# Performance work log

Measured on AMD Instinct MI355X. Metric: run time of the kernel, lower is better.

## Reference

```python
import jax, jax.numpy as jnp
import numpy as np

FP4_E2M1_VALUES = [0.0, 0.0625, 8.0, 1.0, 2.0, 3.0, 4.0, 6.0,
                   -0.0, -0.0625, -8.0, -1.0, -2.0, -3.0, -4.0, -6.0]

M, N, K = 4096, 4096, 4096


def setup_inputs() -> dict:
    key = jax.random.key(0)
    k1, k2 = jax.random.split(key)
    x = jax.random.normal(k1, (M, K), dtype=jnp.float16)
    # packed uint8 bytes stored as int32 (values in [0,256)); each byte holds
    # two fp4 indices: high nibble = even k, low nibble = odd k
    packed_weight = jax.random.randint(k2, (N, K // 2), 0, 256, dtype=jnp.int32)
    lut = jnp.array(FP4_E2M1_VALUES, dtype=jnp.float16)
    return {"x": x, "packed_weight": packed_weight, "lut": lut}


def reference(x, packed_weight, lut):
    # Dequantize: unpack nibbles along K, LUT lookup -> W [N, K] fp16
    n, kh = packed_weight.shape
    high = (packed_weight >> 4) & 15   # even k positions
    low = packed_weight & 15           # odd k positions
    idx = jnp.stack([high, low], axis=-1).reshape(n, 2 * kh)  # [N, K]
    w = lut[idx]                       # [N, K] fp16
    # GEMM with fp32 accumulation (Triton kernel accumulates in fp32), cast to fp16
    y = jnp.einsum('mk,nk->mn', x, w, preferred_element_type=jnp.float32)
    return y.astype(jnp.float16)
```

## Files before the change

kernel.cpp:

```cpp
#include <hip/hip_runtime.h>
#include <hip/hip_fp16.h>
#include <stdint.h>

#define M_DIM 4096
#define N_DIM 4096
#define K_DIM 4096
#define BM 128
#define BN 128
#define BK 32
#define KW (K_DIM / 2)
#define WS_XH_BYTES ((size_t)M_DIM * K_DIM * 2)
#define WS_WH_BYTES ((size_t)N_DIM * K_DIM * 2)

typedef _Float16 half8 __attribute__((ext_vector_type(8)));
typedef float f32x4 __attribute__((ext_vector_type(4)));

__device__ __forceinline__ uint32_t pk2(float a, float b) {
  auto h = __builtin_amdgcn_cvt_pkrtz(a, b);
  return __builtin_bit_cast(uint32_t, h);
}

__device__ __forceinline__ uint32_t dq(uint32_t b, uint32_t ph, uint32_t pl) {
#if __has_builtin(__builtin_amdgcn_perm)
  const uint32_t sel = ((b & 0x70u) << 4) | ((b & 0x07u) << 24);
  uint32_t v = __builtin_amdgcn_perm(ph, pl, sel);
#else
  const uint64_t pool = ((uint64_t)ph << 32) | pl;
  const uint32_t mh = (uint32_t)(pool >> (((b >> 4) & 7u) * 8)) & 0xFFu;
  const uint32_t ml = (uint32_t)(pool >> ((b & 7u) * 8)) & 0xFFu;
  uint32_t v = (mh << 8) | (ml << 24);
#endif
  const uint32_t sg = ((b & 0x88u) * 0x10000100u) & 0x80008000u;
  return v | sg;
}

__device__ __forceinline__ void lut_pool(const float* __restrict__ lutf,
                                         uint32_t& ph, uint32_t& pl) {
  const uint32_t h01 = pk2(lutf[0], lutf[1]);
  const uint32_t h23 = pk2(lutf[2], lutf[3]);
  const uint32_t h45 = pk2(lutf[4], lutf[5]);
  const uint32_t h67 = pk2(lutf[6], lutf[7]);
#if __has_builtin(__builtin_amdgcn_perm)
  pl = __builtin_amdgcn_perm(h23, h01, 0x07050301u);
  ph = __builtin_amdgcn_perm(h67, h45, 0x07050301u);
#else
  pl = ((h01 >> 8) & 0xFFu) | ((h01 >> 24) << 8) |
       (((h23 >> 8) & 0xFFu) << 16) | ((h23 >> 24) << 24);
  ph = ((h45 >> 8) & 0xFFu) | ((h45 >> 24) << 8) |
       (((h67 >> 8) & 0xFFu) << 16) | ((h67 >> 24) << 24);
#endif
}

__global__ __launch_bounds__(256) void cvt_x_kernel(const float4* __restrict__ xin,
                                                    uint4* __restrict__ xout) {
  const int i = blockIdx.x * 256 + threadIdx.x;
  const float4 v0 = xin[2 * i];
  const float4 v1 = xin[2 * i + 1];
  xout[i] = make_uint4(pk2(v0.x, v0.y), pk2(v0.z, v0.w),
                       pk2(v1.x, v1.y), pk2(v1.z, v1.w));
}

__global__ __launch_bounds__(256) void wdq_kernel(const int4* __restrict__ pin,
                                                  uint4* __restrict__ wout,
                                                  const float* __restrict__ lutf) {
  uint32_t ph, pl;
  lut_pool(lutf, ph, pl);
  const int i = blockIdx.x * 256 + threadIdx.x;
  const int4 w = pin[i];
  wout[i] = make_uint4(dq(w.x, ph, pl), dq(w.y, ph, pl),
                       dq(w.z, ph, pl), dq(w.w, ph, pl));
}

__global__ __launch_bounds__(256, 2) void f16gemm_kernel(
    const uint8_t* __restrict__ xh,
    const uint8_t* __restrict__ wh,
    float* __restrict__ out)
{
  __shared__ uint16_t ldsA[BM * BK];
  __shared__ uint16_t ldsB[BN * BK];

  const int tid  = threadIdx.x;
  const int lane = tid & 63;
  const int wave = tid >> 6;
  const int wm   = wave >> 1;
  const int wn   = wave & 1;
  const int m0 = blockIdx.y * BM;
  const int n0 = blockIdx.x * BN;

  f32x4 acc[4][4];
#pragma unroll
  for (int i = 0; i < 4; ++i)
#pragma unroll
    for (int j = 0; j < 4; ++j) acc[i][j] = (f32x4){0.f, 0.f, 0.f, 0.f};

  const uint8_t* xbase = xh + (size_t)m0 * K_DIM * 2;
  const uint8_t* wbase = wh + (size_t)n0 * K_DIM * 2;

  for (int kt = 0; kt < K_DIM / BK; ++kt) {
    __syncthreads();

#pragma unroll
    for (int s = 0; s < 2; ++s) {
      const int idx = tid + s * 256;
      const int row = idx >> 2;
      const int c16 = idx & 3;
      const int g16 = c16 ^ ((row >> 1) & 3);
      const size_t goff = ((size_t)row * K_DIM + kt * BK) * 2 + g16 * 16;
      __builtin_amdgcn_global_load_lds(
          (const __attribute__((address_space(1))) uint32_t*)(xbase + goff),
          (__attribute__((address_space(3))) uint32_t*)((uint8_t*)ldsA + (size_t)idx * 16),
          16, 0, 0);
      __builtin_amdgcn_global_load_lds(
          (const __attribute__((address_space(1))) uint32_t*)(wbase + goff),
          (__attribute__((address_space(3))) uint32_t*)((uint8_t*)ldsB + (size_t)idx * 16),
          16, 0, 0);
    }

    __syncthreads();

    const int q = lane >> 4;
    half8 af[4], bfr[4];
#pragma unroll
    for (int i = 0; i < 4; ++i) {
      const int row = wm * 64 + i * 16 + (lane & 15);
      const uint16_t* pa = ldsA + row * BK + (q ^ ((row >> 1) & 3)) * 8;
      af[i] = *(const half8*)pa;
    }
#pragma unroll
    for (int j = 0; j < 4; ++j) {
      const int row = wn * 64 + j * 16 + (lane & 15);
      const uint16_t* pb = ldsB + row * BK + (q ^ ((row >> 1) & 3)) * 8;
      bfr[j] = *(const half8*)pb;
    }
#pragma unroll
    for (int i = 0; i < 4; ++i)
#pragma unroll
      for (int j = 0; j < 4; ++j)
        acc[i][j] = __builtin_amdgcn_mfma_f32_16x16x32_f16(af[i], bfr[j], acc[i][j], 0, 0, 0);
  }

  const int mb = m0 + wm * 64 + (lane >> 4) * 4;
  const int nb = n0 + wn * 64 + (lane & 15);
#pragma unroll
  for (int i = 0; i < 4; ++i)
#pragma unroll
    for (int j = 0; j < 4; ++j)
#pragma unroll
      for (int r = 0; r < 4; ++r)
        out[(size_t)(mb + i * 16 + r) * N_DIM + (nb + j * 16)] = acc[i][j][r];
}

__global__ __launch_bounds__(256, 2) void fp4gemm_kernel(
    const uint8_t* __restrict__ xh,
    const int* __restrict__ pw,
    const float* __restrict__ lutf,
    float* __restrict__ out)
{
  __shared__ uint16_t ldsA[BM * BK];
  __shared__ uint16_t ldsB[BN * BK];

  const int tid  = threadIdx.x;
  const int lane = tid & 63;
  const int wave = tid >> 6;
  const int wm   = wave >> 1;
  const int wn   = wave & 1;
  const int m0 = blockIdx.y * BM;
  const int n0 = blockIdx.x * BN;

  uint32_t ph, pl;
  lut_pool(lutf, ph, pl);

  f32x4 acc[4][4];
#pragma unroll
  for (int i = 0; i < 4; ++i)
#pragma unroll
    for (int j = 0; j < 4; ++j) acc[i][j] = (f32x4){0.f, 0.f, 0.f, 0.f};

  const int rowB  = tid >> 1;
  const int halfB = tid & 1;
  const int swzB  = (rowB >> 1) & 3;

  for (int kt = 0; kt < K_DIM / BK; ++kt) {
    __syncthreads();

#pragma unroll
    for (int s = 0; s < 2; ++s) {
      const int idx = tid + s * 256;
      const int row = idx >> 2;
      const int c16 = idx & 3;
      const int g16 = c16 ^ ((row >> 1) & 3);
      const uint8_t* gp = xh + ((size_t)(m0 + row) * K_DIM + kt * BK) * 2 + g16 * 16;
      uint8_t* lp = (uint8_t*)ldsA + (size_t)idx * 16;
      __builtin_amdgcn_global_load_lds(
          (const __attribute__((address_space(1))) uint32_t*)gp,
          (__attribute__((address_space(3))) uint32_t*)lp, 16, 0, 0);
    }

    {
      const int* gp = pw + (size_t)(n0 + rowB) * KW + kt * (BK / 2) + halfB * 8;
      const int4 wA = ((const int4*)gp)[0];
      const int4 wB = ((const int4*)gp)[1];
      uint8_t* base = (uint8_t*)ldsB + rowB * 64;
      *(uint4*)(base + ((halfB * 2 + 0) ^ swzB) * 16) =
          make_uint4(dq(wA.x, ph, pl), dq(wA.y, ph, pl),
                     dq(wA.z, ph, pl), dq(wA.w, ph, pl));
      *(uint4*)(base + ((halfB * 2 + 1) ^ swzB) * 16) =
          make_uint4(dq(wB.x, ph, pl), dq(wB.y, ph, pl),
                     dq(wB.z, ph, pl), dq(wB.w, ph, pl));
    }

    __syncthreads();

    const int q = lane >> 4;
    half8 af[4], bfr[4];
#pragma unroll
    for (int i = 0; i < 4; ++i) {
      const int row = wm * 64 + i * 16 + (lane & 15);
      const uint16_t* pa = ldsA + row * BK + (q ^ ((row >> 1) & 3)) * 8;
      af[i] = *(const half8*)pa;
    }
#pragma unroll
    for (int j = 0; j < 4; ++j) {
      const int row = wn * 64 + j * 16 + (lane & 15);
      const uint16_t* pb = ldsB + row * BK + (q ^ ((row >> 1) & 3)) * 8;
      bfr[j] = *(const half8*)pb;
    }
#pragma unroll
    for (int i = 0; i < 4; ++i)
#pragma unroll
      for (int j = 0; j < 4; ++j)
        acc[i][j] = __builtin_amdgcn_mfma_f32_16x16x32_f16(af[i], bfr[j], acc[i][j], 0, 0, 0);
  }

  const int mb = m0 + wm * 64 + (lane >> 4) * 4;
  const int nb = n0 + wn * 64 + (lane & 15);
#pragma unroll
  for (int i = 0; i < 4; ++i)
#pragma unroll
    for (int j = 0; j < 4; ++j)
#pragma unroll
      for (int r = 0; r < 4; ++r)
        out[(size_t)(mb + i * 16 + r) * N_DIM + (nb + j * 16)] = acc[i][j][r];
}

extern "C" void kernel_launch(void* const* d_in, const int* in_sizes, int n_in,
                              void* d_out, int out_size, void* d_ws, size_t ws_size,
                              hipStream_t stream) {
  const void* px = nullptr; const void* ppw = nullptr; const void* plut = nullptr;
  for (int i = 0; i < n_in; ++i) {
    const long s = in_sizes[i];
    if (s == (long)M_DIM * K_DIM) px = d_in[i];
    else if (s == (long)N_DIM * KW) ppw = d_in[i];
    else if (s == 16) plut = d_in[i];
  }
  if (!px || !ppw || !plut) { px = d_in[0]; ppw = d_in[1]; plut = d_in[2]; }

  dim3 grid(N_DIM / BN, M_DIM / BM);

  cvt_x_kernel<<<(M_DIM * K_DIM / 8) / 256, 256, 0, stream>>>(
      (const float4*)px, (uint4*)d_ws);

  if (ws_size >= WS_XH_BYTES + WS_WH_BYTES) {
    uint8_t* wh = (uint8_t*)d_ws + WS_XH_BYTES;
    wdq_kernel<<<(N_DIM * KW / 4) / 256, 256, 0, stream>>>(
        (const int4*)ppw, (uint4*)wh, (const float*)plut);
    f16gemm_kernel<<<grid, dim3(256), 0, stream>>>(
        (const uint8_t*)d_ws, wh, (float*)d_out);
  } else {
    fp4gemm_kernel<<<grid, dim3(256), 0, stream>>>(
        (const uint8_t*)d_ws, (const int*)ppw, (const float*)plut, (float*)d_out);
  }
}
```

Measured before the change: 295.8 us.

## Replace fp16 GEMM with 256x256 tile, double-buffered, pipelined 8-wave kernel

```diff
diff --git a/kernel.cpp b/kernel.cpp
--- a/kernel.cpp
+++ b/kernel.cpp
@@ -5,9 +5,6 @@
 #define M_DIM 4096
 #define N_DIM 4096
 #define K_DIM 4096
-#define BM 128
-#define BN 128
-#define BK 32
 #define KW (K_DIM / 2)
 #define WS_XH_BYTES ((size_t)M_DIM * K_DIM * 2)
 #define WS_WH_BYTES ((size_t)N_DIM * K_DIM * 2)
@@ -71,90 +68,183 @@
                        dq(w.z, ph, pl), dq(w.w, ph, pl));
 }
 
-__global__ __launch_bounds__(256, 2) void f16gemm_kernel(
+__device__ __forceinline__ f32x4 mfma16(half8 a, half8 b, f32x4 c) {
+  return __builtin_amdgcn_mfma_f32_16x16x32_f16(a, b, c, 0, 0, 0);
+}
+
+#define NT (K_DIM / 64)
+
+__global__ __launch_bounds__(512, 2) void f16gemm256_kernel(
     const uint8_t* __restrict__ xh,
     const uint8_t* __restrict__ wh,
     float* __restrict__ out)
 {
-  __shared__ uint16_t ldsA[BM * BK];
-  __shared__ uint16_t ldsB[BN * BK];
+  __shared__ uint16_t Al[2][2][256 * 32];
+  __shared__ uint16_t Bl[2][2][256 * 32];
 
   const int tid  = threadIdx.x;
   const int lane = tid & 63;
   const int wave = tid >> 6;
-  const int wm   = wave >> 1;
-  const int wn   = wave & 1;
-  const int m0 = blockIdx.y * BM;
-  const int n0 = blockIdx.x * BN;
-
-  f32x4 acc[4][4];
-#pragma unroll
-  for (int i = 0; i < 4; ++i)
+  const int wm   = wave >> 2;
+  const int wn   = wave & 3;
+
+  const int bid = blockIdx.x;
+  const int sw  = (bid & 7) * 32 + (bid >> 3);
+  const int m0  = (sw >> 4) * 256;
+  const int n0  = (sw & 15) * 256;
+
+  const uint8_t* asrc[2];
+  const uint8_t* bsrc[2];
+  int ldst[2];
+#pragma unroll
+  for (int s = 0; s < 2; ++s) {
+    const int slot = tid + s * 512;
+    const int row  = slot >> 2;
+    const int g    = (slot & 3) ^ ((row >> 1) & 3);
+    asrc[s] = xh + ((size_t)(m0 + row) * K_DIM) * 2 + g * 16;
+    bsrc[s] = wh + ((size_t)(n0 + row) * K_DIM) * 2 + g * 16;
+    ldst[s] = slot * 16;
+  }
+
+  auto STAGE = [&](int isB, int buf, int kh, int tt) {
+    const int koff  = tt * 128 + kh * 64;
+    uint8_t* lb = (uint8_t*)(isB ? &Bl[0][0][0] : &Al[0][0][0]) +
+                  (buf * 2 + kh) * 16384;
+#pragma unroll
+    for (int s = 0; s < 2; ++s) {
+      const uint8_t* gp = (isB ? bsrc[s] : asrc[s]) + koff;
+      __builtin_amdgcn_global_load_lds(
+          (const __attribute__((address_space(1))) uint32_t*)gp,
+          (__attribute__((address_space(3))) uint32_t*)(lb + ldst[s]), 16, 0, 0);
+    }
+  };
+
+  int aoff[8], boff[4];
+#pragma unroll
+  for (int m = 0; m < 8; ++m) {
+    const int row = wm * 128 + m * 16 + (lane & 15);
+    const int ch  = (lane >> 4) ^ ((row >> 1) & 3);
+    aoff[m] = row * 32 + ch * 8;
+  }
+#pragma unroll
+  for (int n = 0; n < 4; ++n) {
+    const int row = wn * 64 + n * 16 + (lane & 15);
+    const int ch  = (lane >> 4) ^ ((row >> 1) & 3);
+    boff[n] = row * 32 + ch * 8;
+  }
+
+  f32x4 acc[8][4];
+#pragma unroll
+  for (int i = 0; i < 8; ++i)
 #pragma unroll
     for (int j = 0; j < 4; ++j) acc[i][j] = (f32x4){0.f, 0.f, 0.f, 0.f};
 
-  const uint8_t* xbase = xh + (size_t)m0 * K_DIM * 2;
-  const uint8_t* wbase = wh + (size_t)n0 * K_DIM * 2;
-
-  for (int kt = 0; kt < K_DIM / BK; ++kt) {
-    __syncthreads();
-
-#pragma unroll
-    for (int s = 0; s < 2; ++s) {
-      const int idx = tid + s * 256;
-      const int row = idx >> 2;
-      const int c16 = idx & 3;
-      const int g16 = c16 ^ ((row >> 1) & 3);
-      const size_t goff = ((size_t)row * K_DIM + kt * BK) * 2 + g16 * 16;
-      __builtin_amdgcn_global_load_lds(
-          (const __attribute__((address_space(1))) uint32_t*)(xbase + goff),
-          (__attribute__((address_space(3))) uint32_t*)((uint8_t*)ldsA + (size_t)idx * 16),
-          16, 0, 0);
-      __builtin_amdgcn_global_load_lds(
-          (const __attribute__((address_space(1))) uint32_t*)(wbase + goff),
-          (__attribute__((address_space(3))) uint32_t*)((uint8_t*)ldsB + (size_t)idx * 16),
-          16, 0, 0);
-    }
-
-    __syncthreads();
-
-    const int q = lane >> 4;
-    half8 af[4], bfr[4];
-#pragma unroll
-    for (int i = 0; i < 4; ++i) {
-      const int row = wm * 64 + i * 16 + (lane & 15);
-      const uint16_t* pa = ldsA + row * BK + (q ^ ((row >> 1) & 3)) * 8;
-      af[i] = *(const half8*)pa;
-    }
-#pragma unroll
-    for (int j = 0; j < 4; ++j) {
-      const int row = wn * 64 + j * 16 + (lane & 15);
-      const uint16_t* pb = ldsB + row * BK + (q ^ ((row >> 1) & 3)) * 8;
-      bfr[j] = *(const half8*)pb;
-    }
-#pragma unroll
-    for (int i = 0; i < 4; ++i)
-#pragma unroll
-      for (int j = 0; j < 4; ++j)
-        acc[i][j] = __builtin_amdgcn_mfma_f32_16x16x32_f16(af[i], bfr[j], acc[i][j], 0, 0, 0);
-  }
-
-  const int mb = m0 + wm * 64 + (lane >> 4) * 4;
+  STAGE(1, 0, 0, 0);
+  STAGE(0, 0, 0, 0);
+  STAGE(1, 0, 1, 0);
+  STAGE(0, 0, 1, 0);
+  STAGE(1, 1, 0, 1);
+  STAGE(0, 1, 0, 1);
+  asm volatile("s_waitcnt vmcnt(8)" ::: "memory");
+  __builtin_amdgcn_s_barrier();
+
+  half8 af[4], bfr[4];
+
+#pragma unroll 2
+  for (int t = 0; t < NT; ++t) {
+    const int cur = t & 1;
+    const uint16_t* Ab = &Al[cur][0][0];
+    const uint16_t* Bb = &Bl[cur][0][0];
+    const bool st1 = (t + 1 < NT);
+    const bool st2 = (t + 2 < NT);
+
+#pragma unroll
+    for (int n = 0; n < 4; ++n) bfr[n] = *(const half8*)(Bb + boff[n]);
+#pragma unroll
+    for (int m = 0; m < 4; ++m) af[m] = *(const half8*)(Ab + aoff[m]);
+    if (st1) STAGE(1, cur ^ 1, 1, t + 1);
+    __builtin_amdgcn_s_barrier();
+    asm volatile("s_waitcnt lgkmcnt(0)" ::: "memory");
+    __builtin_amdgcn_sched_barrier(0);
+    __builtin_amdgcn_s_setprio(1);
+#pragma unroll
+    for (int m = 0; m < 4; ++m)
+#pragma unroll
+      for (int n = 0; n < 4; ++n)
+        acc[m][n] = mfma16(af[m], bfr[n], acc[m][n]);
+    __builtin_amdgcn_s_setprio(0);
+    __builtin_amdgcn_s_barrier();
+
+#pragma unroll
+    for (int m = 0; m < 4; ++m) af[m] = *(const half8*)(Ab + aoff[4 + m]);
+    if (st1) STAGE(0, cur ^ 1, 1, t + 1);
+    __builtin_amdgcn_s_barrier();
+    asm volatile("s_waitcnt lgkmcnt(0)" ::: "memory");
+    __builtin_amdgcn_sched_barrier(0);
+    __builtin_amdgcn_s_setprio(1);
+#pragma unroll
+    for (int m = 0; m < 4; ++m)
+#pragma unroll
+      for (int n = 0; n < 4; ++n)
+        acc[4 + m][n] = mfma16(af[m], bfr[n], acc[4 + m][n]);
+    __builtin_amdgcn_s_setprio(0);
+    if (st1) asm volatile("s_waitcnt vmcnt(8)" ::: "memory");
+    else     asm volatile("s_waitcnt vmcnt(0)" ::: "memory");
+    __builtin_amdgcn_s_barrier();
+
+#pragma unroll
+    for (int n = 0; n < 4; ++n) bfr[n] = *(const half8*)(Bb + 8192 + boff[n]);
+#pragma unroll
+    for (int m = 0; m < 4; ++m) af[m] = *(const half8*)(Ab + 8192 + aoff[m]);
+    if (st2) STAGE(1, cur, 0, t + 2);
+    __builtin_amdgcn_s_barrier();
+    asm volatile("s_waitcnt lgkmcnt(0)" ::: "memory");
+    __builtin_amdgcn_sched_barrier(0);
+    __builtin_amdgcn_s_setprio(1);
+#pragma unroll
+    for (int m = 0; m < 4; ++m)
+#pragma unroll
+      for (int n = 0; n < 4; ++n)
+        acc[m][n] = mfma16(af[m], bfr[n], acc[m][n]);
+    __builtin_amdgcn_s_setprio(0);
+    __builtin_amdgcn_s_barrier();
+
+#pragma unroll
+    for (int m = 0; m < 4; ++m) af[m] = *(const half8*)(Ab + 8192 + aoff[4 + m]);
+    if (st2) STAGE(0, cur, 0, t + 2);
+    __builtin_amdgcn_s_barrier();
+    asm volatile("s_waitcnt lgkmcnt(0)" ::: "memory");
+    __builtin_amdgcn_sched_barrier(0);
+    __builtin_amdgcn_s_setprio(1);
+#pragma unroll
+    for (int m = 0; m < 4; ++m)
+#pragma unroll
+      for (int n = 0; n < 4; ++n)
+        acc[4 + m][n] = mfma16(af[m], bfr[n], acc[4 + m][n]);
+    __builtin_amdgcn_s_setprio(0);
+    if (st2)      asm volatile("s_waitcnt vmcnt(8)" ::: "memory");
+    else if (st1) asm volatile("s_waitcnt vmcnt(4)" ::: "memory");
+    __builtin_amdgcn_s_barrier();
+  }
+
+  const int mb = m0 + wm * 128 + (lane >> 4) * 4;
   const int nb = n0 + wn * 64 + (lane & 15);
 #pragma unroll
-  for (int i = 0; i < 4; ++i)
-#pragma unroll
-    for (int j = 0; j < 4; ++j)
+  for (int m = 0; m < 8; ++m)
+#pragma unroll
+    for (int n = 0; n < 4; ++n)
 #pragma unroll
       for (int r = 0; r < 4; ++r)
-        out[(size_t)(mb + i * 16 + r) * N_DIM + (nb + j * 16)] = acc[i][j][r];
-}
+        out[(size_t)(mb + m * 16 + r) * N_DIM + (nb + n * 16)] = acc[m][n][r];
+}
+
+#define BM 128
+#define BN 128
+#define BK 32
 
 __global__ __launch_bounds__(256, 2) void fp4gemm_kernel(
-    const uint8_t* __restrict__ xh,
-    const int* __restrict__ pw,
-    const float* __restrict__ lutf,
-    float* __restrict__ out)
+    const uint8_t* __restrict__ xh, const int* __restrict__ pw,
+    const float* __restrict__ lutf, float* __restrict__ out)
 {
   __shared__ uint16_t ldsA[BM * BK];
   __shared__ uint16_t ldsB[BN * BK];
@@ -216,14 +306,12 @@
 #pragma unroll
     for (int i = 0; i < 4; ++i) {
       const int row = wm * 64 + i * 16 + (lane & 15);
-      const uint16_t* pa = ldsA + row * BK + (q ^ ((row >> 1) & 3)) * 8;
-      af[i] = *(const half8*)pa;
+      af[i] = *(const half8*)(ldsA + row * BK + (q ^ ((row >> 1) & 3)) * 8);
     }
 #pragma unroll
     for (int j = 0; j < 4; ++j) {
       const int row = wn * 64 + j * 16 + (lane & 15);
-      const uint16_t* pb = ldsB + row * BK + (q ^ ((row >> 1) & 3)) * 8;
-      bfr[j] = *(const half8*)pb;
+      bfr[j] = *(const half8*)(ldsB + row * BK + (q ^ ((row >> 1) & 3)) * 8);
     }
 #pragma unroll
     for (int i = 0; i < 4; ++i)
@@ -255,8 +343,6 @@
   }
   if (!px || !ppw || !plut) { px = d_in[0]; ppw = d_in[1]; plut = d_in[2]; }
 
-  dim3 grid(N_DIM / BN, M_DIM / BM);
-
   cvt_x_kernel<<<(M_DIM * K_DIM / 8) / 256, 256, 0, stream>>>(
       (const float4*)px, (uint4*)d_ws);
 
@@ -264,9 +350,10 @@
     uint8_t* wh = (uint8_t*)d_ws + WS_XH_BYTES;
     wdq_kernel<<<(N_DIM * KW / 4) / 256, 256, 0, stream>>>(
         (const int4*)ppw, (uint4*)wh, (const float*)plut);
-    f16gemm_kernel<<<grid, dim3(256), 0, stream>>>(
+    f16gemm256_kernel<<<dim3(256), dim3(512), 0, stream>>>(
         (const uint8_t*)d_ws, wh, (float*)d_out);
   } else {
+    dim3 grid(N_DIM / BN, M_DIM / BM);
     fp4gemm_kernel<<<grid, dim3(256), 0, stream>>>(
         (const uint8_t*)d_ws, (const int*)ppw, (const float*)plut, (float*)d_out);
   }
```

New measurement: 268.9 us. -9.1%, faster.
